# Kernel tuning notes

Hardware: AMD Instinct MI355X
Metric: run time of the kernel (lower is better)

Reference implementation:

```python
import jax, jax.numpy as jnp
import numpy as np

B, NQ, S, H, NH = 2, 1024, 4096, 1024, 16
HD = H // NH
EPS = 1e-6


def layer_norm(x, gamma, beta):
    mu = jnp.mean(x, axis=-1, keepdims=True)
    var = jnp.mean(jnp.square(x - mu), axis=-1, keepdims=True)
    return (x - mu) * jax.lax.rsqrt(var + EPS) * gamma + beta


def setup_inputs() -> dict:
    key = jax.random.key(0)
    ks = jax.random.split(key, 6)
    queries = jax.random.normal(ks[0], (B, NQ, H), dtype=jnp.float32)
    keys_values = jax.random.normal(ks[1], (B, S, H), dtype=jnp.float32)
    attention_mask = jax.random.uniform(ks[2], (B, S)) > 0.1
    attention_mask = attention_mask.at[:, 0].set(True)
    # params (torch Linear stored transposed here so y = x @ W + b)
    W_qkv = jax.random.normal(ks[3], (H, 3 * H), dtype=jnp.float32) * 0.02
    b_qkv = jnp.zeros((3 * H,), dtype=jnp.float32)
    W_out = jax.random.normal(ks[4], (H, H), dtype=jnp.float32) * 0.02
    b_out = jnp.zeros((H,), dtype=jnp.float32)
    gamma = jnp.ones((H,), dtype=jnp.float32)
    beta = jnp.zeros((H,), dtype=jnp.float32)
    return {"queries": queries, "keys_values": keys_values,
            "attention_mask": attention_mask,
            "W_qkv": W_qkv, "b_qkv": b_qkv, "W_out": W_out, "b_out": b_out,
            "gamma": gamma, "beta": beta}


def reference(queries, keys_values, attention_mask, W_qkv, b_qkv, W_out, b_out, gamma, beta):
    # shared LayerNorm + shared qkv projection applied to both streams
    q_in = layer_norm(queries, gamma, beta)
    kv_in = layer_norm(keys_values, gamma, beta)
    q = (q_in @ W_qkv + b_qkv)[..., :H]                    # [B,NQ,H]
    kv = kv_in @ W_qkv + b_qkv
    k = kv[..., H:2 * H]                                    # [B,S,H]
    v = kv[..., 2 * H:]                                     # [B,S,H]
    q = q.reshape(B, NQ, NH, HD)
    k = k.reshape(B, S, NH, HD)
    v = v.reshape(B, S, NH, HD)
    scale = 1.0 / np.sqrt(HD).astype(np.float32)
    scores = jnp.einsum('bqhd,bkhd->bhqk', q, k) * scale    # [B,NH,NQ,S]
    neg_inf = jnp.finfo(scores.dtype).min
    scores = jnp.where(attention_mask[:, None, None, :], scores, neg_inf)
    attn = jax.nn.softmax(scores, axis=-1)
    out = jnp.einsum('bhqk,bkhd->bqhd', attn, v).reshape(B, NQ, H)
    return out @ W_out + b_out
```

## Files before the change

### kernel.cpp

```cpp
#include <hip/hip_runtime.h>
#include <stdint.h>

#define DEVI __device__ __forceinline__

constexpr int Bb = 2, NQ = 1024, S = 4096, H = 1024, NH = 16, HD = 64;
constexpr int NSPLIT = 4, SLEN = S / NSPLIT;

typedef __bf16 bf16x8 __attribute__((ext_vector_type(8)));
typedef float f32x4 __attribute__((ext_vector_type(4)));
typedef int i32x4 __attribute__((ext_vector_type(4)));
typedef unsigned short u16;
typedef u16 u16x8 __attribute__((ext_vector_type(8)));

DEVI u16 f2bf(float f) {
  union { float f; unsigned u; } v; v.f = f;
  unsigned r = (v.u + 0x7fffu + ((v.u >> 16) & 1u)) >> 16;
  return (u16)r;
}

DEVI float bf2f(u16 x) {
  union { unsigned u; float f; } v; v.u = ((unsigned)x) << 16;
  return v.f;
}

DEVI float fexp2(float x) {
#if __has_builtin(__builtin_amdgcn_exp2f)
  return __builtin_amdgcn_exp2f(x);
#else
  return exp2f(x);
#endif
}

DEVI void gload_lds16(const void* g, void* lds) {
  __builtin_amdgcn_global_load_lds(
      (const __attribute__((address_space(1))) void*)(uintptr_t)g,
      (__attribute__((address_space(3))) void*)(uint32_t)(uintptr_t)lds,
      16, 0, 0);
}

DEVI void ln_body(const float* __restrict__ x, const float* __restrict__ gamma,
                  const float* __restrict__ beta, u16* __restrict__ out, int row) {
  int lane = threadIdx.x & 63;
  const float4* xr = (const float4*)(x + (size_t)row * H);
  float4 v[4];
  float s = 0.f, s2 = 0.f;
#pragma unroll
  for (int i = 0; i < 4; ++i) {
    v[i] = xr[lane + i * 64];
    s += v[i].x + v[i].y + v[i].z + v[i].w;
    s2 += v[i].x * v[i].x + v[i].y * v[i].y + v[i].z * v[i].z + v[i].w * v[i].w;
  }
#pragma unroll
  for (int d = 1; d < 64; d <<= 1) { s += __shfl_xor(s, d); s2 += __shfl_xor(s2, d); }
  float mu = s * (1.f / H);
  float rstd = rsqrtf(s2 * (1.f / H) - mu * mu + 1e-6f);
  u16* orow = out + (size_t)row * H;
  const float4* g4 = (const float4*)gamma;
  const float4* b4 = (const float4*)beta;
#pragma unroll
  for (int i = 0; i < 4; ++i) {
    float4 g = g4[lane + i * 64], bb = b4[lane + i * 64];
    ushort4 o;
    o.x = f2bf((v[i].x - mu) * rstd * g.x + bb.x);
    o.y = f2bf((v[i].y - mu) * rstd * g.y + bb.y);
    o.z = f2bf((v[i].z - mu) * rstd * g.z + bb.z);
    o.w = f2bf((v[i].w - mu) * rstd * g.w + bb.w);
    *(ushort4*)(orow + (size_t)(lane + i * 64) * 4) = o;
  }
}

__global__ __launch_bounds__(256) void prep_kernel(
    const unsigned char* __restrict__ mraw, unsigned char* __restrict__ maskN,
    const float* __restrict__ queries, const float* __restrict__ keys_values,
    const float* __restrict__ gamma, const float* __restrict__ beta,
    u16* __restrict__ Xq, u16* __restrict__ Xkv,
    const float* __restrict__ W_qkv, const float* __restrict__ W_out,
    u16* __restrict__ Wtq, u16* __restrict__ Wto) {
  __shared__ int isByte;
  __shared__ float tile[32][33];
  const int b = blockIdx.x;
  if (b == 0) {
    if (threadIdx.x == 0) isByte = 0;
    __syncthreads();
    int any = 0;
    for (int p = threadIdx.x; p < Bb * S; p += 256)
      if ((p & 3) && mraw[p]) any = 1;
    if (any) atomicOr(&isByte, 1);
    __syncthreads();
    const int bytemode = isByte;
    for (int i = threadIdx.x; i < Bb * S; i += 256) {
      unsigned char v = bytemode ? (unsigned char)(mraw[i] != 0)
                                 : (unsigned char)(((const int*)mraw)[i] != 0);
      maskN[i] = v;
    }
  } else if (b < 513) {
    ln_body(queries, gamma, beta, Xq, (b - 1) * 4 + (threadIdx.x >> 6));
  } else if (b < 2561) {
    ln_body(keys_values, gamma, beta, Xkv, (b - 513) * 4 + (threadIdx.x >> 6));
  } else {
    const float* in; u16* out; int C, t;
    if (b < 5633) { t = b - 2561; in = W_qkv; out = Wtq; C = 3 * H; }
    else          { t = b - 5633; in = W_out; out = Wto; C = H; }
    const int nbx = C / 32;
    int c0 = (t % nbx) * 32, r0 = (t / nbx) * 32;
    int tx = threadIdx.x & 31, ty = threadIdx.x >> 5;
#pragma unroll
    for (int i = 0; i < 32; i += 8)
      tile[ty + i][tx] = in[(size_t)(r0 + ty + i) * C + c0 + tx];
    __syncthreads();
#pragma unroll
    for (int i = 0; i < 32; i += 8)
      out[(size_t)(c0 + ty + i) * H + r0 + tx] = f2bf(tile[tx][ty + i]);
  }
}

__global__ __launch_bounds__(512, 2) void gemm_kvq_kernel(
    const u16* __restrict__ Xkv, const u16* __restrict__ Xq,
    const u16* __restrict__ Wtq, const float* __restrict__ b_qkv,
    u16* __restrict__ KVbuf, u16* __restrict__ Qbuf) {
  __shared__ __align__(16) u16 Abuf[4][256 * 32];
  __shared__ __align__(16) u16 Bbuf[4][256 * 32];
  const int tid = threadIdx.x, wid = tid >> 6, lane = tid & 63;
  const int fr = lane & 15, fq = lane >> 4;
  const int wr = (wid >> 2) * 128, wc = (wid & 3) * 64;
  const int bid = blockIdx.x;
  const bool isQ = bid >= 256;
  int by, bx;
  const u16 *Ap, *Bp;
  const float* bias;
  if (!isQ) {
    const int xcd = bid & 7, loc = bid >> 3;
    by = xcd * 4 + (loc & 3); bx = loc >> 2;
    Ap = Xkv; Bp = Wtq + (size_t)H * H; bias = b_qkv + H;
  } else {
    const int t = bid - 256;
    by = t >> 2; bx = t & 3;
    Ap = Xq; Bp = Wtq; bias = b_qkv;
  }
  const u16* Ag = Ap + (size_t)(by * 256) * 1024;
  const u16* Bg = Bp + (size_t)(bx * 256) * 1024;

  f32x4 acc[8][4] = {};

  auto stage = [&](int tt) {
    const int k0 = tt * 32;
    u16* Ad = &Abuf[tt & 3][0];
    u16* Bd = &Bbuf[tt & 3][0];
#pragma unroll
    for (int l = 0; l < 2; ++l) {
      int ci = tid + l * 512;
      int row = ci >> 2, ch = ci & 3;
      int chs = ch ^ ((row >> 1) & 3);
      gload_lds16(Ag + (size_t)row * 1024 + k0 + chs * 8, Ad + ci * 8);
      gload_lds16(Bg + (size_t)row * 1024 + k0 + chs * 8, Bd + ci * 8);
    }
  };

#define KV_ITER(T, VM)                                                          \
  {                                                                             \
    asm volatile("s_waitcnt vmcnt(" #VM ")" ::: "memory");                      \
    __syncthreads();                                                            \
    const u16* Ac = &Abuf[(T) & 3][0];                                          \
    const u16* Bc = &Bbuf[(T) & 3][0];                                          \
    bf16x8 af[8], bfv[4];                                                       \
    _Pragma("unroll") for (int m = 0; m < 8; ++m) {                             \
      int row = wr + m * 16 + fr;                                               \
      af[m] = *(const bf16x8*)(Ac + row * 32 + (fq ^ ((row >> 1) & 3)) * 8);    \
    }                                                                           \
    _Pragma("unroll") for (int n = 0; n < 4; ++n) {                             \
      int row = wc + n * 16 + fr;                                               \
      bfv[n] = *(const bf16x8*)(Bc + row * 32 + (fq ^ ((row >> 1) & 3)) * 8);   \
    }                                                                           \
    if ((T) + 3 < 32) stage((T) + 3);                                           \
    __builtin_amdgcn_s_setprio(1);                                              \
    _Pragma("unroll") for (int m = 0; m < 8; ++m)                               \
      _Pragma("unroll") for (int n = 0; n < 4; ++n)                             \
        acc[m][n] = __builtin_amdgcn_mfma_f32_16x16x32_bf16(af[m], bfv[n], acc[m][n], 0, 0, 0); \
    __builtin_amdgcn_s_setprio(0);                                              \
  }

  stage(0);
  stage(1);
  stage(2);
  for (int t = 0; t < 29; ++t) KV_ITER(t, 8)
  KV_ITER(29, 8)
  KV_ITER(30, 4)
  KV_ITER(31, 0)
#undef KV_ITER

  constexpr float QSCALE = 0.125f * 1.4426950408889634f;
#pragma unroll
  for (int m = 0; m < 8; ++m)
#pragma unroll
    for (int n = 0; n < 4; ++n) {
      const int c = bx * 256 + wc + n * 16 + fr;
      const int r0 = by * 256 + wr + m * 16 + fq * 4;
      const float bv = bias[c];
      if (isQ) {
#pragma unroll
        for (int i = 0; i < 4; ++i) {
          int r = r0 + i;
          Qbuf[((((size_t)(r >> 10)) * NH + (c >> 6)) * NQ + (r & (NQ - 1))) * HD + (c & 63)] =
              f2bf((acc[m][n][i] + bv) * QSCALE);
        }
      } else if (c >= 1024) {
        int bb = r0 >> 12, kv = r0 & (S - 1);
        int cc = c - 1024, head = cc >> 6, d = cc & 63;
        ushort4 o;
        o.x = f2bf(acc[m][n][0] + bv);
        o.y = f2bf(acc[m][n][1] + bv);
        o.z = f2bf(acc[m][n][2] + bv);
        o.w = f2bf(acc[m][n][3] + bv);
        u16* vb = KVbuf + (size_t)Bb * NH * S * HD;
        *(ushort4*)(vb + (((size_t)(bb * NH + head)) * HD + d) * S + kv) = o;
      } else {
#pragma unroll
        for (int i = 0; i < 4; ++i) {
          int r = r0 + i;
          KVbuf[((((size_t)(r >> 12)) * NH + (c >> 6)) * S + (r & (S - 1))) * HD + (c & 63)] =
              f2bf(acc[m][n][i] + bv);
        }
      }
    }
}

__global__ __launch_bounds__(256, 2) void gemm_out_kernel(
    const u16* __restrict__ A, const u16* __restrict__ Bt,
    const float* __restrict__ bias, float* __restrict__ outp) {
  __shared__ __align__(16) u16 Abuf[4][128 * 32];
  __shared__ __align__(16) u16 Bbuf[4][128 * 32];
  const int tid = threadIdx.x, wid = tid >> 6, lane = tid & 63;
  const int fr = lane & 15, fq = lane >> 4;
  const int wr = (wid >> 1) * 64, wc = (wid & 1) * 64;
  const int brow = blockIdx.y * 128, bcol = blockIdx.x * 128;
  const u16* Ag = A + (size_t)brow * 1024;
  const u16* Bg = Bt + (size_t)bcol * 1024;

  f32x4 acc[4][4] = {};

  auto stage = [&](int tt) {
    const int k0 = tt * 32;
    u16* Ad = &Abuf[tt & 3][0];
    u16* Bd = &Bbuf[tt & 3][0];
#pragma unroll
    for (int l = 0; l < 2; ++l) {
      int ci = tid + l * 256;
      int row = ci >> 2, ch = ci & 3;
      int chs = ch ^ ((row >> 1) & 3);
      gload_lds16(Ag + (size_t)row * 1024 + k0 + chs * 8, Ad + ci * 8);
      gload_lds16(Bg + (size_t)row * 1024 + k0 + chs * 8, Bd + ci * 8);
    }
  };

#define OUT_ITER(T, VM)                                                         \
  {                                                                             \
    asm volatile("s_waitcnt vmcnt(" #VM ")" ::: "memory");                      \
    __syncthreads();                                                            \
    const u16* Ac = &Abuf[(T) & 3][0];                                          \
    const u16* Bc = &Bbuf[(T) & 3][0];                                          \
    bf16x8 af[4], bfv[4];                                                       \
    _Pragma("unroll") for (int m = 0; m < 4; ++m) {                             \
      int row = wr + m * 16 + fr;                                               \
      af[m] = *(const bf16x8*)(Ac + row * 32 + (fq ^ ((row >> 1) & 3)) * 8);    \
    }                                                                           \
    _Pragma("unroll") for (int n = 0; n < 4; ++n) {                             \
      int row = wc + n * 16 + fr;                                               \
      bfv[n] = *(const bf16x8*)(Bc + row * 32 + (fq ^ ((row >> 1) & 3)) * 8);   \
    }                                                                           \
    if ((T) + 3 < 32) stage((T) + 3);                                           \
    __builtin_amdgcn_s_setprio(1);                                              \
    _Pragma("unroll") for (int m = 0; m < 4; ++m)                               \
      _Pragma("unroll") for (int n = 0; n < 4; ++n)                             \
        acc[m][n] = __builtin_amdgcn_mfma_f32_16x16x32_bf16(af[m], bfv[n], acc[m][n], 0, 0, 0); \
    __builtin_amdgcn_s_setprio(0);                                              \
  }

  stage(0);
  stage(1);
  stage(2);
  for (int t = 0; t < 29; ++t) OUT_ITER(t, 8)
  OUT_ITER(29, 8)
  OUT_ITER(30, 4)
  OUT_ITER(31, 0)
#undef OUT_ITER

#pragma unroll
  for (int m = 0; m < 4; ++m)
#pragma unroll
    for (int n = 0; n < 4; ++n) {
      const int c = bcol + wc + n * 16 + fr;
      const int r0 = brow + wr + m * 16 + fq * 4;
#pragma unroll
      for (int i = 0; i < 4; ++i)
        outp[(size_t)(r0 + i) * H + c] = acc[m][n][i] + bias[c];
    }
}

__global__ __launch_bounds__(512, 4) void attn_kernel(
    const u16* __restrict__ Qb, const u16* __restrict__ Kb,
    const u16* __restrict__ Vt, const unsigned char* __restrict__ mask,
    u16* __restrict__ Opart, float2* __restrict__ ml) {
  __shared__ __align__(16) char smem[34816];
  u16* Ktile = (u16*)smem;
  u16* Vtile = Ktile + 8192;
  float* Mb = (float*)(Vtile + 8192);
  const int bflat = blockIdx.x;
  const int r = bflat & 7, idx = bflat >> 3;
  const int q0 = (idx & 3) * 256;
  const int g = (idx >> 2) * 8 + r;
  const int bh = g & 31, z = g >> 5;
  const int b = bh >> 4, kv0 = z * SLEN;
  const int tid = threadIdx.x, w = tid >> 6, lane = tid & 63;
  const int fr = lane & 15, fq = lane >> 4, fr7 = fr & 7;
  const u16* QgA = Qb + ((size_t)bh * NQ + q0 + w * 32) * HD;
  const u16* QgB = QgA + 16 * HD;
  const u16* Kg = Kb + (size_t)bh * S * HD;
  const u16* Vg = Vt + (size_t)bh * HD * S;
  const unsigned char* mg = mask + (size_t)b * S + kv0;

  const int rs = tid >> 3, gs = (tid & 7) ^ (rs & 7);

  bf16x8 qfA0 = *(const bf16x8*)(QgA + fr * HD + fq * 8);
  bf16x8 qfA1 = *(const bf16x8*)(QgA + fr * HD + 32 + fq * 8);
  bf16x8 qfB0 = *(const bf16x8*)(QgB + fr * HD + fq * 8);
  bf16x8 qfB1 = *(const bf16x8*)(QgB + fr * HD + 32 + fq * 8);

  const int A0 = ((((fq << 1)) & 3) * 16 + fr) << 2;
  const int A1 = ((((fq << 1) + 1) & 3) * 16 + fr) << 2;
  const bool lofq = (fq < 2);

  f32x4 oaccA[4] = {}, oaccB[4] = {};
  float mrowA = -1e30f, lrowA = 0.f, mrowB = -1e30f, lrowB = 0.f;

  if (tid < 64) Mb[tid] = mg[tid] ? 0.f : -1e30f;
  gload_lds16(Kg + (size_t)(kv0 + rs) * HD + gs * 8, Ktile + tid * 8);
  gload_lds16(Vg + (size_t)rs * S + kv0 + gs * 8, Vtile + tid * 8);
  asm volatile("s_waitcnt vmcnt(0)" ::: "memory");
  __syncthreads();

  int cur = 0;
  for (int kt = 0; kt < SLEN; kt += 64) {
    const int nb = cur ^ 1, kn = kt + 64;
    if (kn < SLEN) {
      if (tid < 64) Mb[nb * 64 + tid] = mg[kn + tid] ? 0.f : -1e30f;
      gload_lds16(Kg + (size_t)(kv0 + kn + rs) * HD + gs * 8, Ktile + nb * 4096 + tid * 8);
      gload_lds16(Vg + (size_t)rs * S + kv0 + kn + gs * 8, Vtile + nb * 4096 + tid * 8);
    }

    const u16* Kc = Ktile + cur * 4096;
    const u16* Vc = Vtile + cur * 4096;

    float svA[4][4], svB[4][4];
    __builtin_amdgcn_s_setprio(1);
#pragma unroll
    for (int nt = 0; nt < 4; ++nt) {
      const u16* kb2 = Kc + (nt * 16 + fr) * 64;
      bf16x8 k0v = *(const bf16x8*)(kb2 + ((fq) ^ fr7) * 8);
      bf16x8 k1v = *(const bf16x8*)(kb2 + ((4 + fq) ^ fr7) * 8);
      f32x4 tA = {}, tB = {};
      tA = __builtin_amdgcn_mfma_f32_16x16x32_bf16(k0v, qfA0, tA, 0, 0, 0);
      tA = __builtin_amdgcn_mfma_f32_16x16x32_bf16(k1v, qfA1, tA, 0, 0, 0);
      tB = __builtin_amdgcn_mfma_f32_16x16x32_bf16(k0v, qfB0, tB, 0, 0, 0);
      tB = __builtin_amdgcn_mfma_f32_16x16x32_bf16(k1v, qfB1, tB, 0, 0, 0);
      float4 mb = *(const float4*)&Mb[cur * 64 + nt * 16 + fq * 4];
      svA[nt][0] = tA[0] + mb.x; svA[nt][1] = tA[1] + mb.y;
      svA[nt][2] = tA[2] + mb.z; svA[nt][3] = tA[3] + mb.w;
      svB[nt][0] = tB[0] + mb.x; svB[nt][1] = tB[1] + mb.y;
      svB[nt][2] = tB[2] + mb.z; svB[nt][3] = tB[3] + mb.w;
    }
    __builtin_amdgcn_s_setprio(0);

    float pmaxA, pmaxB;
    {
      float a0 = fmaxf(fmaxf(svA[0][0], svA[0][1]), fmaxf(svA[0][2], svA[0][3]));
      float a1 = fmaxf(fmaxf(svA[1][0], svA[1][1]), fmaxf(svA[1][2], svA[1][3]));
      float a2 = fmaxf(fmaxf(svA[2][0], svA[2][1]), fmaxf(svA[2][2], svA[2][3]));
      float a3 = fmaxf(fmaxf(svA[3][0], svA[3][1]), fmaxf(svA[3][2], svA[3][3]));
      pmaxA = fmaxf(fmaxf(a0, a1), fmaxf(a2, a3));
      float b0 = fmaxf(fmaxf(svB[0][0], svB[0][1]), fmaxf(svB[0][2], svB[0][3]));
      float b1 = fmaxf(fmaxf(svB[1][0], svB[1][1]), fmaxf(svB[1][2], svB[1][3]));
      float b2 = fmaxf(fmaxf(svB[2][0], svB[2][1]), fmaxf(svB[2][2], svB[2][3]));
      float b3 = fmaxf(fmaxf(svB[3][0], svB[3][1]), fmaxf(svB[3][2], svB[3][3]));
      pmaxB = fmaxf(fmaxf(b0, b1), fmaxf(b2, b3));
    }
    if (__any(pmaxA > mrowA + 12.f)) {
      pmaxA = fmaxf(pmaxA, __shfl_xor(pmaxA, 16));
      pmaxA = fmaxf(pmaxA, __shfl_xor(pmaxA, 32));
      float nm = fmaxf(mrowA, pmaxA);
      float al = fexp2(mrowA - nm);
      mrowA = nm; lrowA *= al;
#pragma unroll
      for (int nt = 0; nt < 4; ++nt)
#pragma unroll
        for (int i = 0; i < 4; ++i) oaccA[nt][i] *= al;
    }
    if (__any(pmaxB > mrowB + 12.f)) {
      pmaxB = fmaxf(pmaxB, __shfl_xor(pmaxB, 16));
      pmaxB = fmaxf(pmaxB, __shfl_xor(pmaxB, 32));
      float nm = fmaxf(mrowB, pmaxB);
      float al = fexp2(mrowB - nm);
      mrowB = nm; lrowB *= al;
#pragma unroll
      for (int nt = 0; nt < 4; ++nt)
#pragma unroll
        for (int i = 0; i < 4; ++i) oaccB[nt][i] *= al;
    }

    float pA[4][4], pB[4][4];
#pragma unroll
    for (int nt = 0; nt < 4; ++nt)
#pragma unroll
      for (int i = 0; i < 4; ++i) {
        pA[nt][i] = fexp2(svA[nt][i] - mrowA);
        pB[nt][i] = fexp2(svB[nt][i] - mrowB);
      }
    {
      float s0 = (pA[0][0] + pA[0][1]) + (pA[0][2] + pA[0][3]);
      float s1 = (pA[1][0] + pA[1][1]) + (pA[1][2] + pA[1][3]);
      float s2 = (pA[2][0] + pA[2][1]) + (pA[2][2] + pA[2][3]);
      float s3 = (pA[3][0] + pA[3][1]) + (pA[3][2] + pA[3][3]);
      lrowA += (s0 + s1) + (s2 + s3);
      float t0 = (pB[0][0] + pB[0][1]) + (pB[0][2] + pB[0][3]);
      float t1 = (pB[1][0] + pB[1][1]) + (pB[1][2] + pB[1][3]);
      float t2 = (pB[2][0] + pB[2][1]) + (pB[2][2] + pB[2][3]);
      float t3 = (pB[3][0] + pB[3][1]) + (pB[3][2] + pB[3][3]);
      lrowB += (t0 + t1) + (t2 + t3);
    }

    int pkA[4][2], pkB[4][2];
#pragma unroll
    for (int nt = 0; nt < 4; ++nt) {
      asm("v_cvt_pk_bf16_f32 %0, %1, %2" : "=v"(pkA[nt][0]) : "v"(pA[nt][0]), "v"(pA[nt][1]));
      asm("v_cvt_pk_bf16_f32 %0, %1, %2" : "=v"(pkA[nt][1]) : "v"(pA[nt][2]), "v"(pA[nt][3]));
      asm("v_cvt_pk_bf16_f32 %0, %1, %2" : "=v"(pkB[nt][0]) : "v"(pB[nt][0]), "v"(pB[nt][1]));
      asm("v_cvt_pk_bf16_f32 %0, %1, %2" : "=v"(pkB[nt][1]) : "v"(pB[nt][2]), "v"(pB[nt][3]));
    }

#pragma unroll
    for (int b2 = 0; b2 < 2; ++b2) {
      i32x4 wvA, wvB;
      {
        int w0a = __builtin_amdgcn_ds_bpermute(A0, pkA[2 * b2][0]);
        int w0b = __builtin_amdgcn_ds_bpermute(A0, pkA[2 * b2 + 1][0]);
        int w1a = __builtin_amdgcn_ds_bpermute(A0, pkA[2 * b2][1]);
        int w1b = __builtin_amdgcn_ds_bpermute(A0, pkA[2 * b2 + 1][1]);
        int w2a = __builtin_amdgcn_ds_bpermute(A1, pkA[2 * b2][0]);
        int w2b = __builtin_amdgcn_ds_bpermute(A1, pkA[2 * b2 + 1][0]);
        int w3a = __builtin_amdgcn_ds_bpermute(A1, pkA[2 * b2][1]);
        int w3b = __builtin_amdgcn_ds_bpermute(A1, pkA[2 * b2 + 1][1]);
        wvA[0] = lofq ? w0a : w0b;
        wvA[1] = lofq ? w1a : w1b;
        wvA[2] = lofq ? w2a : w2b;
        wvA[3] = lofq ? w3a : w3b;
      }
      {
        int w0a = __builtin_amdgcn_ds_bpermute(A0, pkB[2 * b2][0]);
        int w0b = __builtin_amdgcn_ds_bpermute(A0, pkB[2 * b2 + 1][0]);
        int w1a = __builtin_amdgcn_ds_bpermute(A0, pkB[2 * b2][1]);
        int w1b = __builtin_amdgcn_ds_bpermute(A0, pkB[2 * b2 + 1][1]);
        int w2a = __builtin_amdgcn_ds_bpermute(A1, pkB[2 * b2][0]);
        int w2b = __builtin_amdgcn_ds_bpermute(A1, pkB[2 * b2 + 1][0]);
        int w3a = __builtin_amdgcn_ds_bpermute(A1, pkB[2 * b2][1]);
        int w3b = __builtin_amdgcn_ds_bpermute(A1, pkB[2 * b2 + 1][1]);
        wvB[0] = lofq ? w0a : w0b;
        wvB[1] = lofq ? w1a : w1b;
        wvB[2] = lofq ? w2a : w2b;
        wvB[3] = lofq ? w3a : w3b;
      }
      bf16x8 pfragA = __builtin_bit_cast(bf16x8, wvA);
      bf16x8 pfragB = __builtin_bit_cast(bf16x8, wvB);
      __builtin_amdgcn_s_setprio(1);
#pragma unroll
      for (int nt = 0; nt < 4; ++nt) {
        const u16* vb2 = Vc + (nt * 16 + fr) * 64;
        bf16x8 vf = *(const bf16x8*)(vb2 + ((b2 * 4 + fq) ^ fr7) * 8);
        oaccA[nt] = __builtin_amdgcn_mfma_f32_16x16x32_bf16(vf, pfragA, oaccA[nt], 0, 0, 0);
        oaccB[nt] = __builtin_amdgcn_mfma_f32_16x16x32_bf16(vf, pfragB, oaccB[nt], 0, 0, 0);
      }
      __builtin_amdgcn_s_setprio(0);
    }

    asm volatile("s_waitcnt vmcnt(0)" ::: "memory");
    __syncthreads();
    cur = nb;
  }

  lrowA += __shfl_xor(lrowA, 16);
  lrowA += __shfl_xor(lrowA, 32);
  lrowB += __shfl_xor(lrowB, 16);
  lrowB += __shfl_xor(lrowB, 32);
  if (fq == 0) {
    ml[((size_t)z * 32 + bh) * NQ + q0 + w * 32 + fr] = float2{mrowA, lrowA};
    ml[((size_t)z * 32 + bh) * NQ + q0 + w * 32 + 16 + fr] = float2{mrowB, lrowB};
  }

  float* tb = (float*)smem + w * 1088;
  const int qloc = lane >> 2, dl = lane & 3;
#pragma unroll
  for (int gsel = 0; gsel < 2; ++gsel) {
    const f32x4* oc = gsel ? oaccB : oaccA;
#pragma unroll
    for (int nt = 0; nt < 4; ++nt)
#pragma unroll
      for (int i = 0; i < 4; ++i)
        tb[fr * 68 + nt * 16 + fq * 4 + i] = oc[nt][i];
    const float* trow = tb + qloc * 68 + dl * 16;
    u16* gdst = Opart +
        (((size_t)z * 32 + bh) * NQ + q0 + w * 32 + gsel * 16 + qloc) * 64 + dl * 16;
    u16x8 o0, o1;
#pragma unroll
    for (int j = 0; j < 8; ++j) {
      o0[j] = f2bf(trow[j]);
      o1[j] = f2bf(trow[8 + j]);
    }
    *(u16x8*)gdst = o0;
    *(u16x8*)(gdst + 8) = o1;
  }
}

__global__ __launch_bounds__(256) void combine_kernel(
    const u16* __restrict__ Opart, const float2* __restrict__ ml,
    u16* __restrict__ out) {
  const int bh = blockIdx.y, b = bh >> 4, h = bh & 15;
  const int q = blockIdx.x * 64 + (threadIdx.x >> 2);
  const int dl = threadIdx.x & 3;
  float2 mm[NSPLIT];
  float M = -1e30f;
#pragma unroll
  for (int zz = 0; zz < NSPLIT; ++zz) {
    mm[zz] = ml[((size_t)zz * 32 + bh) * NQ + q];
    M = fmaxf(M, mm[zz].x);
  }
  float wz[NSPLIT], lsum = 0.f;
#pragma unroll
  for (int zz = 0; zz < NSPLIT; ++zz) {
    wz[zz] = fexp2(mm[zz].x - M);
    lsum += mm[zz].y * wz[zz];
  }
  const float inv = 1.f / lsum;
  float acc[16] = {};
#pragma unroll
  for (int zz = 0; zz < NSPLIT; ++zz) {
    const u16* op = Opart + (((size_t)zz * 32 + bh) * NQ + q) * 64 + dl * 16;
    u16x8 a0 = *(const u16x8*)op;
    u16x8 a1 = *(const u16x8*)(op + 8);
    float wi = wz[zz] * inv;
#pragma unroll
    for (int j = 0; j < 8; ++j) {
      acc[j] += wi * bf2f(a0[j]);
      acc[8 + j] += wi * bf2f(a1[j]);
    }
  }
  u16* orow = out + ((size_t)b * NQ + q) * H + h * HD + dl * 16;
  u16x8 o0, o1;
#pragma unroll
  for (int j = 0; j < 8; ++j) {
    o0[j] = f2bf(acc[j]);
    o1[j] = f2bf(acc[8 + j]);
  }
  *(u16x8*)orow = o0;
  *(u16x8*)(orow + 8) = o1;
}

extern "C" void kernel_launch(void* const* d_in, const int* in_sizes, int n_in,
                              void* d_out, int out_size, void* d_ws, size_t ws_size,
                              hipStream_t stream) {
  const float* queries = (const float*)d_in[0];
  const float* keys_values = (const float*)d_in[1];
  const void* amask = d_in[2];
  const float* W_qkv = (const float*)d_in[3];
  const float* b_qkv = (const float*)d_in[4];
  const float* W_out = (const float*)d_in[5];
  const float* b_out = (const float*)d_in[6];
  const float* gamma = (const float*)d_in[7];
  const float* beta = (const float*)d_in[8];

  char* ws = (char*)d_ws;
  unsigned char* maskN = (unsigned char*)ws;
  u16* Xq = (u16*)(ws + 8192);
  u16* Xkv = Xq + (size_t)Bb * NQ * H;
  u16* Wtq = Xkv + (size_t)Bb * S * H;
  u16* Wto = Wtq + (size_t)3 * H * H;
  u16* Qbuf = Wto + (size_t)H * H;
  u16* Kbuf = Qbuf + (size_t)Bb * NQ * H;
  u16* Aout = Kbuf + (size_t)2 * Bb * S * H;
  u16* Opart = (u16*)(ws + 8192);
  float2* ml = (float2*)((char*)Opart + (size_t)NSPLIT * 32 * NQ * 64 * 2);

  hipLaunchKernelGGL(prep_kernel, dim3(6657), dim3(256), 0, stream,
                     (const unsigned char*)amask, maskN, queries, keys_values,
                     gamma, beta, Xq, Xkv, W_qkv, W_out, Wtq, Wto);
  hipLaunchKernelGGL(gemm_kvq_kernel, dim3(288), dim3(512), 0, stream,
                     Xkv, Xq, Wtq, b_qkv, Kbuf, Qbuf);
  hipLaunchKernelGGL(attn_kernel, dim3(NQ / 256 * Bb * NH * NSPLIT), dim3(512), 0, stream,
                     Qbuf, Kbuf, Kbuf + (size_t)Bb * S * H, maskN, Opart, ml);
  hipLaunchKernelGGL(combine_kernel, dim3(NQ / 64, Bb * NH), dim3(256), 0, stream,
                     Opart, ml, Aout);
  hipLaunchKernelGGL(gemm_out_kernel, dim3(H / 128, Bb * NQ / 128), dim3(256), 0, stream,
                     Aout, Wto, b_out, (float*)d_out);
}
```

Measured before the change: 169.6 us.

## Split Q projection out of fused KV GEMM into separate 128-tile GEMM

Removes the Q-projection blocks from the large 256x256-tile KV GEMM so that kernel launches exactly 256 blocks. The Q projection now runs through a templated 128x128-tile GEMM shared with the output projection, with a Q-specific epilogue. The intent is to avoid a tail wave of large Q tiles running after the KV tiles. The cost is an extra kernel launch and a serial dependency between the two GEMMs.

```diff
diff --git a/kernel.cpp b/kernel.cpp
--- a/kernel.cpp
+++ b/kernel.cpp
@@ -114,31 +114,19 @@
   }
 }
 
-__global__ __launch_bounds__(512, 2) void gemm_kvq_kernel(
-    const u16* __restrict__ Xkv, const u16* __restrict__ Xq,
-    const u16* __restrict__ Wtq, const float* __restrict__ b_qkv,
-    u16* __restrict__ KVbuf, u16* __restrict__ Qbuf) {
+__global__ __launch_bounds__(512, 2) void gemm_kv_kernel(
+    const u16* __restrict__ Xkv, const u16* __restrict__ WtqKV,
+    const float* __restrict__ bias, u16* __restrict__ KVbuf) {
   __shared__ __align__(16) u16 Abuf[4][256 * 32];
   __shared__ __align__(16) u16 Bbuf[4][256 * 32];
   const int tid = threadIdx.x, wid = tid >> 6, lane = tid & 63;
   const int fr = lane & 15, fq = lane >> 4;
   const int wr = (wid >> 2) * 128, wc = (wid & 3) * 64;
   const int bid = blockIdx.x;
-  const bool isQ = bid >= 256;
-  int by, bx;
-  const u16 *Ap, *Bp;
-  const float* bias;
-  if (!isQ) {
-    const int xcd = bid & 7, loc = bid >> 3;
-    by = xcd * 4 + (loc & 3); bx = loc >> 2;
-    Ap = Xkv; Bp = Wtq + (size_t)H * H; bias = b_qkv + H;
-  } else {
-    const int t = bid - 256;
-    by = t >> 2; bx = t & 3;
-    Ap = Xq; Bp = Wtq; bias = b_qkv;
-  }
-  const u16* Ag = Ap + (size_t)(by * 256) * 1024;
-  const u16* Bg = Bp + (size_t)(bx * 256) * 1024;
+  const int xcd = bid & 7, loc = bid >> 3;
+  const int by = xcd * 4 + (loc & 3), bx = loc >> 2;
+  const u16* Ag = Xkv + (size_t)(by * 256) * 1024;
+  const u16* Bg = WtqKV + (size_t)(bx * 256) * 1024;
 
   f32x4 acc[8][4] = {};
 
@@ -188,7 +176,6 @@
   KV_ITER(31, 0)
 #undef KV_ITER
 
-  constexpr float QSCALE = 0.125f * 1.4426950408889634f;
 #pragma unroll
   for (int m = 0; m < 8; ++m)
 #pragma unroll
@@ -196,14 +183,7 @@
       const int c = bx * 256 + wc + n * 16 + fr;
       const int r0 = by * 256 + wr + m * 16 + fq * 4;
       const float bv = bias[c];
-      if (isQ) {
-#pragma unroll
-        for (int i = 0; i < 4; ++i) {
-          int r = r0 + i;
-          Qbuf[((((size_t)(r >> 10)) * NH + (c >> 6)) * NQ + (r & (NQ - 1))) * HD + (c & 63)] =
-              f2bf((acc[m][n][i] + bv) * QSCALE);
-        }
-      } else if (c >= 1024) {
+      if (c >= 1024) {
         int bb = r0 >> 12, kv = r0 & (S - 1);
         int cc = c - 1024, head = cc >> 6, d = cc & 63;
         ushort4 o;
@@ -224,9 +204,10 @@
     }
 }
 
-__global__ __launch_bounds__(256, 2) void gemm_out_kernel(
+template <int EPI>
+__global__ __launch_bounds__(256, 2) void gemm128_kernel(
     const u16* __restrict__ A, const u16* __restrict__ Bt,
-    const float* __restrict__ bias, float* __restrict__ outp) {
+    const float* __restrict__ bias, void* __restrict__ outp) {
   __shared__ __align__(16) u16 Abuf[4][128 * 32];
   __shared__ __align__(16) u16 Bbuf[4][128 * 32];
   const int tid = threadIdx.x, wid = tid >> 6, lane = tid & 63;
@@ -284,6 +265,7 @@
   OUT_ITER(31, 0)
 #undef OUT_ITER
 
+  constexpr float QSCALE = 0.125f * 1.4426950408889634f;
 #pragma unroll
   for (int m = 0; m < 4; ++m)
 #pragma unroll
@@ -291,8 +273,17 @@
       const int c = bcol + wc + n * 16 + fr;
       const int r0 = brow + wr + m * 16 + fq * 4;
 #pragma unroll
-      for (int i = 0; i < 4; ++i)
-        outp[(size_t)(r0 + i) * H + c] = acc[m][n][i] + bias[c];
+      for (int i = 0; i < 4; ++i) {
+        int r = r0 + i;
+        float val = acc[m][n][i] + bias[c];
+        if constexpr (EPI == 0) {
+          u16* qb = (u16*)outp;
+          qb[((((size_t)(r >> 10)) * NH + (c >> 6)) * NQ + (r & (NQ - 1))) * HD + (c & 63)] =
+              f2bf(val * QSCALE);
+        } else {
+          ((float*)outp)[(size_t)r * H + c] = val;
+        }
+      }
     }
 }
 
@@ -590,12 +581,14 @@
   hipLaunchKernelGGL(prep_kernel, dim3(6657), dim3(256), 0, stream,
                      (const unsigned char*)amask, maskN, queries, keys_values,
                      gamma, beta, Xq, Xkv, W_qkv, W_out, Wtq, Wto);
-  hipLaunchKernelGGL(gemm_kvq_kernel, dim3(288), dim3(512), 0, stream,
-                     Xkv, Xq, Wtq, b_qkv, Kbuf, Qbuf);
+  hipLaunchKernelGGL(gemm_kv_kernel, dim3(256), dim3(512), 0, stream,
+                     Xkv, Wtq + (size_t)H * H, b_qkv + H, Kbuf);
+  hipLaunchKernelGGL(gemm128_kernel<0>, dim3(8, 16), dim3(256), 0, stream,
+                     Xq, Wtq, b_qkv, (void*)Qbuf);
   hipLaunchKernelGGL(attn_kernel, dim3(NQ / 256 * Bb * NH * NSPLIT), dim3(512), 0, stream,
                      Qbuf, Kbuf, Kbuf + (size_t)Bb * S * H, maskN, Opart, ml);
   hipLaunchKernelGGL(combine_kernel, dim3(NQ / 64, Bb * NH), dim3(256), 0, stream,
                      Opart, ml, Aout);
-  hipLaunchKernelGGL(gemm_out_kernel, dim3(H / 128, Bb * NQ / 128), dim3(256), 0, stream,
-                     Aout, Wto, b_out, (float*)d_out);
-}
+  hipLaunchKernelGGL(gemm128_kernel<1>, dim3(8, 16), dim3(256), 0, stream,
+                     Aout, Wto, b_out, (void*)d_out);
+}
```

Result: faster. 162.1 us (-4.4%).
